# Kernel optimization log

Measured on AMD Instinct MI355X. Metric: run time of the kernel, lower is better.

The kernel has to match this reference:

```python
import jax, jax.numpy as jnp
import numpy as np

IN_F = 512
OUT_F = 512
ALPHA = 0.2   # LeakyReLU negative slope
NEG_INF = -9e15


def setup_inputs() -> dict:
    key = jax.random.key(0)
    k1, k2, k3, k4 = jax.random.split(key, 4)
    B, S = 8, 2048
    hidden_state = jax.random.normal(k1, (B, S, IN_F), dtype=jnp.float32)
    adjacent_matrix = jax.random.uniform(k2, (B, S, S), dtype=jnp.float32)
    # nn.Linear weight (no bias): stored as [out, in] in torch; we keep [in, out] for x @ W
    bound = 1.0 / np.sqrt(IN_F)
    W = jax.random.uniform(k3, (IN_F, OUT_F), dtype=jnp.float32, minval=-bound, maxval=bound)
    # xavier_uniform with gain=1.414 on a: shape [2*out, 1]
    a_bound = 1.414 * np.sqrt(6.0 / (2 * OUT_F + 1))
    a = jax.random.uniform(k4, (2 * OUT_F, 1), dtype=jnp.float32, minval=-a_bound, maxval=a_bound)
    return {"hidden_state": hidden_state, "adjacent_matrix": adjacent_matrix, "W": W, "a": a}


def reference(hidden_state, adjacent_matrix, W, a):
    # Wh: [B, S, out]
    Wh = jnp.einsum('bsi,io->bso', hidden_state, W)
    # additive attention: Wh1 + Wh2^T -> [B, S, S]
    Wh1 = Wh @ a[:OUT_F, :]            # [B, S, 1]
    Wh2 = Wh @ a[OUT_F:, :]            # [B, S, 1]
    e = Wh1 + jnp.swapaxes(Wh2, 1, 2)  # [B, S, S]
    e = jax.nn.leaky_relu(e, negative_slope=ALPHA)
    attention = jnp.where(adjacent_matrix > 0.5, e, NEG_INF)
    # NOTE: original softmaxes over dim=1 (the *row* index), faithfully reproduced
    attention = jax.nn.softmax(attention, axis=1)
    # dropout is identity at inference (training=False)
    h_prime = jnp.einsum('bst,bto->bso', attention, Wh)
    return jax.nn.elu(h_prime)  # concat=True path
```

## Files before the change

### kernel.cpp

```cpp
#include <hip/hip_runtime.h>
#include <hip/hip_bf16.h>
#include <stdint.h>

#define SDIM 2048
#define BDIM 8
#define FDIM 512
constexpr float ALPHA = 0.2f;

typedef __attribute__((ext_vector_type(8))) short bf16x8;
typedef __attribute__((ext_vector_type(4))) float f32x4;

__device__ __forceinline__ unsigned short f2bf(float x) {
  __hip_bfloat16 h = __float2bfloat16(x);
  return *reinterpret_cast<unsigned short*>(&h);
}

__device__ __forceinline__ void gload_lds16(const void* g, void* l) {
  __builtin_amdgcn_global_load_lds(
      (const __attribute__((address_space(1))) unsigned int*)(uintptr_t)g,
      (__attribute__((address_space(3))) unsigned int*)(uintptr_t)l,
      16, 0, 0);
}

__global__ void k0_prep(const float* __restrict__ W, const float* __restrict__ a,
                        float* __restrict__ wa, __hip_bfloat16* __restrict__ WT) {
  int i = blockIdx.x;
  int lane = threadIdx.x;
  float s1 = 0.f, s2 = 0.f;
  for (int o = lane; o < FDIM; o += 64) {
    float w = W[i * FDIM + o];
    s1 += w * a[o];
    s2 += w * a[FDIM + o];
    WT[o * FDIM + i] = __float2bfloat16(w);
  }
  #pragma unroll
  for (int off = 32; off > 0; off >>= 1) {
    s1 += __shfl_down(s1, off);
    s2 += __shfl_down(s2, off);
  }
  if (lane == 0) { wa[i] = s1; wa[FDIM + i] = s2; }
}

__global__ __launch_bounds__(256) void k1_rows(const float* __restrict__ H,
                                               const float* __restrict__ wa,
                                               float* __restrict__ Wh1, float* __restrict__ Wh2,
                                               __hip_bfloat16* __restrict__ Hb) {
  int wid = threadIdx.x >> 6, lane = threadIdx.x & 63;
  long r = (long)blockIdx.x * 4 + wid;
  const float* hr = H + r * FDIM;
  float4 v0 = ((const float4*)hr)[lane];
  float4 v1 = ((const float4*)hr)[lane + 64];
  float4 wa10 = ((const float4*)wa)[lane];
  float4 wa11 = ((const float4*)wa)[lane + 64];
  float4 wa20 = ((const float4*)(wa + FDIM))[lane];
  float4 wa21 = ((const float4*)(wa + FDIM))[lane + 64];
  float s1 = v0.x*wa10.x + v0.y*wa10.y + v0.z*wa10.z + v0.w*wa10.w
           + v1.x*wa11.x + v1.y*wa11.y + v1.z*wa11.z + v1.w*wa11.w;
  float s2 = v0.x*wa20.x + v0.y*wa20.y + v0.z*wa20.z + v0.w*wa20.w
           + v1.x*wa21.x + v1.y*wa21.y + v1.z*wa21.z + v1.w*wa21.w;
  ushort4 u0 = { f2bf(v0.x), f2bf(v0.y), f2bf(v0.z), f2bf(v0.w) };
  ushort4 u1 = { f2bf(v1.x), f2bf(v1.y), f2bf(v1.z), f2bf(v1.w) };
  ushort4* hb = (ushort4*)(Hb + r * FDIM);
  hb[lane] = u0;
  hb[lane + 64] = u1;
  #pragma unroll
  for (int off = 32; off > 0; off >>= 1) {
    s1 += __shfl_down(s1, off);
    s2 += __shfl_down(s2, off);
  }
  if (lane == 0) { Wh1[r] = s1; Wh2[r] = s2; }
}

__global__ __launch_bounds__(256) void k2_z(const float* __restrict__ adj,
                                            const float* __restrict__ Wh1,
                                            const float* __restrict__ Wh2,
                                            float* __restrict__ Zp) {
  int t = blockIdx.x * 256 + threadIdx.x;
  int b = blockIdx.y;
  int c = blockIdx.z;
  float w2 = Wh2[b * SDIM + t];
  const float* arow = adj + ((long)b * SDIM + c * 64) * SDIM + t;
  const float* w1p = Wh1 + b * SDIM + c * 64;
  float z = 0.f;
  #pragma unroll 8
  for (int s = 0; s < 64; ++s) {
    float av = arow[(long)s * SDIM];
    float e = w1p[s] + w2;
    e = e > 0.f ? e : ALPHA * e;
    float p = __expf(e);
    z += (av > 0.5f) ? p : 0.f;
  }
  Zp[(b * 32 + c) * SDIM + t] = z;
}

__global__ void k2b_rz(const float* __restrict__ Zp, float* __restrict__ rZ) {
  int idx = blockIdx.x * 256 + threadIdx.x;
  int b = idx >> 11, t = idx & 2047;
  float z = 0.f;
  #pragma unroll
  for (int c = 0; c < 32; ++c) z += Zp[(b * 32 + c) * SDIM + t];
  rZ[idx] = 1.0f / z;
}

__global__ __launch_bounds__(256) void k3_gemm(const __hip_bfloat16* __restrict__ WTm,
                                               const __hip_bfloat16* __restrict__ Hb,
                                               const float* __restrict__ rZ,
                                               __hip_bfloat16* __restrict__ VT) {
  __shared__ __align__(16) __hip_bfloat16 Asm[2][128 * 32];
  __shared__ __align__(16) __hip_bfloat16 Bsm[2][128 * 32];
  const int o0 = blockIdx.x * 128;
  const int t0 = blockIdx.y * 128;
  const int b = blockIdx.z;
  const int tid = threadIdx.x;
  const int w = tid >> 6, lane = tid & 63;
  const int wm = w >> 1, wn = w & 1;
  const int fr = lane & 15, fq = lane >> 4;
  const int lr = lane >> 2, lb = (lane & 3) * 16;

  const __hip_bfloat16* Abase = WTm + (long)o0 * FDIM;
  const __hip_bfloat16* Bbase = Hb + ((long)b * SDIM + t0) * FDIM;

  f32x4 acc[4][4] = {};

  auto stage = [&](int kk, int buf) {
    #pragma unroll
    for (int g = 0; g < 2; ++g) {
      int rbase = g * 64 + w * 16;
      int row = rbase + lr;
      gload_lds16((const char*)(Abase + (long)row * FDIM + kk * 32) + lb,
                  (char*)&Asm[buf][0] + rbase * 64);
      gload_lds16((const char*)(Bbase + (long)row * FDIM + kk * 32) + lb,
                  (char*)&Bsm[buf][0] + rbase * 64);
    }
  };

  stage(0, 0);
  __syncthreads();
  for (int kk = 0; kk < 16; ++kk) {
    int cur = kk & 1;
    if (kk < 15) stage(kk + 1, cur ^ 1);
    bf16x8 af[4], bf_[4];
    #pragma unroll
    for (int mf = 0; mf < 4; ++mf)
      af[mf] = *(const bf16x8*)((const char*)&Asm[cur][0] + (wm * 64 + mf * 16 + fr) * 64 + fq * 16);
    #pragma unroll
    for (int nf = 0; nf < 4; ++nf)
      bf_[nf] = *(const bf16x8*)((const char*)&Bsm[cur][0] + (wn * 64 + nf * 16 + fr) * 64 + fq * 16);
    #pragma unroll
    for (int mf = 0; mf < 4; ++mf)
      #pragma unroll
      for (int nf = 0; nf < 4; ++nf)
        acc[mf][nf] = __builtin_amdgcn_mfma_f32_16x16x32_bf16(af[mf], bf_[nf], acc[mf][nf], 0, 0, 0);
    __syncthreads();
  }

  #pragma unroll
  for (int nf = 0; nf < 4; ++nf) {
    int t = t0 + wn * 64 + nf * 16 + fr;
    float rz = rZ[b * SDIM + t];
    #pragma unroll
    for (int mf = 0; mf < 4; ++mf) {
      #pragma unroll
      for (int r = 0; r < 4; ++r) {
        int o = o0 + wm * 64 + mf * 16 + fq * 4 + r;
        VT[((long)(b * FDIM + o)) * SDIM + t] = __float2bfloat16(acc[mf][nf][r] * rz);
      }
    }
  }
}

__global__ __launch_bounds__(256, 2) void k4_pv(const float* __restrict__ adj,
                                                const float* __restrict__ Wh1,
                                                const float* __restrict__ Wh2,
                                                const __hip_bfloat16* __restrict__ VT,
                                                float* __restrict__ out) {
  __shared__ __align__(16) __hip_bfloat16 Psm[2][64 * 32];
  __shared__ __align__(16) float w2l[SDIM];
  const int b  = blockIdx.x;
  const int s0 = blockIdx.y * 64;
  const int ob = blockIdx.z * 256;
  const int tid = threadIdx.x;
  const int w = tid >> 6, lane = tid & 63;
  const int fr = lane & 15, fq = lane >> 4;

  const float w1 = Wh1[b * SDIM + s0 + w * 16 + fr];
  const float* adjR = adj + ((long)(b * SDIM + s0 + w * 16 + fr)) * SDIM;
  const __hip_bfloat16* vbase = VT + ((long)(b * FDIM + ob + w * 64 + fr)) * SDIM;

  f32x4 acc[4][4] = {};

  auto loadA = [&](int pp, float4& a0, float4& a1) {
    const float* s = adjR + pp * 32 + fq * 8;
    a0 = *(const float4*)s;
    a1 = *(const float4*)(s + 4);
  };
  auto build = [&](int pp, int pbuf, const float4& a0, const float4& a1) {
    const float* wrow = &w2l[pp * 32 + fq * 8];
    float4 q0 = *(const float4*)(wrow);
    float4 q1 = *(const float4*)(wrow + 4);
    float aa[8] = {a0.x,a0.y,a0.z,a0.w,a1.x,a1.y,a1.z,a1.w};
    float qq[8] = {q0.x,q0.y,q0.z,q0.w,q1.x,q1.y,q1.z,q1.w};
    bf16x8 pv;
    #pragma unroll
    for (int i = 0; i < 8; ++i) {
      float e = w1 + qq[i];
      e = fmaxf(e, ALPHA * e);
      float pr = (aa[i] > 0.5f) ? __expf(e) : 0.f;
      pv[i] = (short)f2bf(pr);
    }
    *(bf16x8*)((char*)&Psm[pbuf][0] + w * 1024 + lane * 16) = pv;
  };

  {
    const float* src = Wh2 + (long)b * SDIM + tid * 8;
    float4 t0 = *(const float4*)(src);
    float4 t1 = *(const float4*)(src + 4);
    *(float4*)(&w2l[tid * 8]) = t0;
    *(float4*)(&w2l[tid * 8 + 4]) = t1;
  }
  float4 a0A, a1A, a0B, a1B, a0C, a1C, a0D, a1D;
  loadA(0, a0A, a1A);
  loadA(1, a0B, a1B);
  loadA(2, a0C, a1C);
  __syncthreads();
  build(0, 0, a0A, a1A);
  asm volatile("s_waitcnt lgkmcnt(0)" ::: "memory");
  __builtin_amdgcn_sched_barrier(0);
  __builtin_amdgcn_s_barrier();

  auto phase = [&](int p, const float4& c0, const float4& c1, float4& f0, float4& f1) {
    const int cur = p & 1;
    bf16x8 vb[4];
    #pragma unroll
    for (int nf = 0; nf < 4; ++nf)
      vb[nf] = *(const bf16x8*)(vbase + (long)nf * 16 * SDIM + p * 32 + fq * 8);
    if (p + 3 < 64) loadA(p + 3, f0, f1);
    __builtin_amdgcn_sched_barrier(0);
    bf16x8 pa[4];
    #pragma unroll
    for (int mf = 0; mf < 4; ++mf)
      pa[mf] = *(const bf16x8*)((const char*)&Psm[cur][0] + mf * 1024 + lane * 16);
    if (p + 1 < 64) build(p + 1, cur ^ 1, c0, c1);
    __builtin_amdgcn_sched_barrier(0);
    __builtin_amdgcn_s_setprio(1);
    #pragma unroll
    for (int mf = 0; mf < 4; ++mf)
      #pragma unroll
      for (int nf = 0; nf < 4; ++nf)
        acc[mf][nf] = __builtin_amdgcn_mfma_f32_16x16x32_bf16(pa[mf], vb[nf], acc[mf][nf], 0, 0, 0);
    __builtin_amdgcn_s_setprio(0);
    asm volatile("s_waitcnt lgkmcnt(0)" ::: "memory");
    __builtin_amdgcn_sched_barrier(0);
    __builtin_amdgcn_s_barrier();
  };

  for (int j = 0; j < 16; ++j) {
    phase(4 * j + 0, a0B, a1B, a0D, a1D);
    phase(4 * j + 1, a0C, a1C, a0A, a1A);
    phase(4 * j + 2, a0D, a1D, a0B, a1B);
    phase(4 * j + 3, a0A, a1A, a0C, a1C);
  }

  float* orow = out + ((long)b * SDIM + s0) * FDIM + ob + w * 64;
  #pragma unroll
  for (int mf = 0; mf < 4; ++mf) {
    #pragma unroll
    for (int nf = 0; nf < 4; ++nf) {
      #pragma unroll
      for (int r = 0; r < 4; ++r) {
        int s = mf * 16 + fq * 4 + r;
        int o = nf * 16 + fr;
        float x = acc[mf][nf][r];
        x = x > 0.f ? x : (__expf(x) - 1.f);
        orow[(long)s * FDIM + o] = x;
      }
    }
  }
}

extern "C" void kernel_launch(void* const* d_in, const int* in_sizes, int n_in,
                              void* d_out, int out_size, void* d_ws, size_t ws_size,
                              hipStream_t stream) {
  const float* H   = (const float*)d_in[0];
  const float* adj = (const float*)d_in[1];
  const float* W   = (const float*)d_in[2];
  const float* a   = (const float*)d_in[3];
  float* out = (float*)d_out;
  char* ws = (char*)d_ws;

  __hip_bfloat16* VT  = (__hip_bfloat16*)(ws + 0);
  __hip_bfloat16* Hb  = (__hip_bfloat16*)(ws + 16777216);
  __hip_bfloat16* WT  = (__hip_bfloat16*)(ws + 33554432);
  float* wa  = (float*)(ws + 34078720);
  float* Wh1 = (float*)(ws + 34082816);
  float* Wh2 = (float*)(ws + 34148352);
  float* rZ  = (float*)(ws + 34213888);
  float* Zp  = (float*)(ws + 34279424);

  hipLaunchKernelGGL(k0_prep, dim3(512), dim3(64), 0, stream, W, a, wa, WT);
  hipLaunchKernelGGL(k1_rows, dim3(4096), dim3(256), 0, stream, H, wa, Wh1, Wh2, Hb);
  hipLaunchKernelGGL(k2_z, dim3(8, 8, 32), dim3(256), 0, stream, adj, Wh1, Wh2, Zp);
  hipLaunchKernelGGL(k2b_rz, dim3(64), dim3(256), 0, stream, Zp, rZ);
  hipLaunchKernelGGL(k3_gemm, dim3(4, 16, 8), dim3(256), 0, stream, WT, Hb, rZ, VT);
  hipLaunchKernelGGL(k4_pv, dim3(8, 32, 2), dim3(256), 0, stream, adj, Wh1, Wh2, VT, out);
}
```

Before: 148.5 us.

## Halve k4_pv row tile to 32 rows, doubling blocks and raising occupancy

The P·V kernel now processes 32 query rows per block instead of 64, which doubles the grid to 1024 blocks and raises launch bounds to 4 blocks per SM. The P-tile build is remapped so each thread computes 4 probabilities for a 32x32 tile, with a new shared-memory layout. The goal is more parallelism and better latency hiding on the adjacency-bound stream. The cost is that each VT tile is reused across only 32 rows, so VT traffic doubles and the w2l staging is repeated in twice as many blocks.

New measurement: 186.5 us. +25.6%, slower.

```diff
diff --git a/kernel.cpp b/kernel.cpp
--- a/kernel.cpp
+++ b/kernel.cpp
@@ -169,46 +169,45 @@
   }
 }
 
-__global__ __launch_bounds__(256, 2) void k4_pv(const float* __restrict__ adj,
+__global__ __launch_bounds__(256, 4) void k4_pv(const float* __restrict__ adj,
                                                 const float* __restrict__ Wh1,
                                                 const float* __restrict__ Wh2,
                                                 const __hip_bfloat16* __restrict__ VT,
                                                 float* __restrict__ out) {
-  __shared__ __align__(16) __hip_bfloat16 Psm[2][64 * 32];
+  __shared__ __align__(16) __hip_bfloat16 Psm[2][32 * 32];
   __shared__ __align__(16) float w2l[SDIM];
   const int b  = blockIdx.x;
-  const int s0 = blockIdx.y * 64;
+  const int s0 = blockIdx.y * 32;
   const int ob = blockIdx.z * 256;
   const int tid = threadIdx.x;
   const int w = tid >> 6, lane = tid & 63;
   const int fr = lane & 15, fq = lane >> 4;
-
-  const float w1 = Wh1[b * SDIM + s0 + w * 16 + fr];
-  const float* adjR = adj + ((long)(b * SDIM + s0 + w * 16 + fr)) * SDIM;
+  const int bfq = tid & 3, bh = (tid >> 2) & 1;
+  const int bfr = (tid >> 3) & 15, bmf = tid >> 7;
+  const int brow = bmf * 16 + bfr;
+
+  const float w1 = Wh1[b * SDIM + s0 + brow];
+  const float* adjR = adj + ((long)(b * SDIM + s0 + brow)) * SDIM;
   const __hip_bfloat16* vbase = VT + ((long)(b * FDIM + ob + w * 64 + fr)) * SDIM;
 
-  f32x4 acc[4][4] = {};
-
-  auto loadA = [&](int pp, float4& a0, float4& a1) {
-    const float* s = adjR + pp * 32 + fq * 8;
-    a0 = *(const float4*)s;
-    a1 = *(const float4*)(s + 4);
+  f32x4 acc[2][4] = {};
+
+  auto loadA = [&](int pp, float4& a0) {
+    a0 = *(const float4*)(adjR + pp * 32 + bfq * 8 + bh * 4);
   };
-  auto build = [&](int pp, int pbuf, const float4& a0, const float4& a1) {
-    const float* wrow = &w2l[pp * 32 + fq * 8];
-    float4 q0 = *(const float4*)(wrow);
-    float4 q1 = *(const float4*)(wrow + 4);
-    float aa[8] = {a0.x,a0.y,a0.z,a0.w,a1.x,a1.y,a1.z,a1.w};
-    float qq[8] = {q0.x,q0.y,q0.z,q0.w,q1.x,q1.y,q1.z,q1.w};
-    bf16x8 pv;
-    #pragma unroll
-    for (int i = 0; i < 8; ++i) {
+  auto build = [&](int pp, int pbuf, const float4& a0) {
+    float4 q0 = *(const float4*)(&w2l[pp * 32 + bfq * 8 + bh * 4]);
+    float aa[4] = {a0.x, a0.y, a0.z, a0.w};
+    float qq[4] = {q0.x, q0.y, q0.z, q0.w};
+    ushort4 pv;
+    #pragma unroll
+    for (int i = 0; i < 4; ++i) {
       float e = w1 + qq[i];
       e = fmaxf(e, ALPHA * e);
       float pr = (aa[i] > 0.5f) ? __expf(e) : 0.f;
-      pv[i] = (short)f2bf(pr);
+      ((unsigned short*)&pv)[i] = f2bf(pr);
     }
-    *(bf16x8*)((char*)&Psm[pbuf][0] + w * 1024 + lane * 16) = pv;
+    *(ushort4*)((char*)&Psm[pbuf][0] + bmf * 1024 + bfr * 64 + bfq * 16 + bh * 8) = pv;
   };
 
   {
@@ -218,33 +217,33 @@
     *(float4*)(&w2l[tid * 8]) = t0;
     *(float4*)(&w2l[tid * 8 + 4]) = t1;
   }
-  float4 a0A, a1A, a0B, a1B, a0C, a1C, a0D, a1D;
-  loadA(0, a0A, a1A);
-  loadA(1, a0B, a1B);
-  loadA(2, a0C, a1C);
+  float4 aA, aB, aC, aD;
+  loadA(0, aA);
+  loadA(1, aB);
+  loadA(2, aC);
   __syncthreads();
-  build(0, 0, a0A, a1A);
+  build(0, 0, aA);
   asm volatile("s_waitcnt lgkmcnt(0)" ::: "memory");
   __builtin_amdgcn_sched_barrier(0);
   __builtin_amdgcn_s_barrier();
 
-  auto phase = [&](int p, const float4& c0, const float4& c1, float4& f0, float4& f1) {
+  auto phase = [&](int p, const float4& c0, float4& f0) {
     const int cur = p & 1;
     bf16x8 vb[4];
     #pragma unroll
     for (int nf = 0; nf < 4; ++nf)
       vb[nf] = *(const bf16x8*)(vbase + (long)nf * 16 * SDIM + p * 32 + fq * 8);
-    if (p + 3 < 64) loadA(p + 3, f0, f1);
+    if (p + 3 < 64) loadA(p + 3, f0);
     __builtin_amdgcn_sched_barrier(0);
-    bf16x8 pa[4];
-    #pragma unroll
-    for (int mf = 0; mf < 4; ++mf)
-      pa[mf] = *(const bf16x8*)((const char*)&Psm[cur][0] + mf * 1024 + lane * 16);
-    if (p + 1 < 64) build(p + 1, cur ^ 1, c0, c1);
+    bf16x8 pa[2];
+    #pragma unroll
+    for (int mf = 0; mf < 2; ++mf)
+      pa[mf] = *(const bf16x8*)((const char*)&Psm[cur][0] + mf * 1024 + fr * 64 + fq * 16);
+    if (p + 1 < 64) build(p + 1, cur ^ 1, c0);
     __builtin_amdgcn_sched_barrier(0);
     __builtin_amdgcn_s_setprio(1);
     #pragma unroll
-    for (int mf = 0; mf < 4; ++mf)
+    for (int mf = 0; mf < 2; ++mf)
       #pragma unroll
       for (int nf = 0; nf < 4; ++nf)
         acc[mf][nf] = __builtin_amdgcn_mfma_f32_16x16x32_bf16(pa[mf], vb[nf], acc[mf][nf], 0, 0, 0);
@@ -255,15 +254,15 @@
   };
 
   for (int j = 0; j < 16; ++j) {
-    phase(4 * j + 0, a0B, a1B, a0D, a1D);
-    phase(4 * j + 1, a0C, a1C, a0A, a1A);
-    phase(4 * j + 2, a0D, a1D, a0B, a1B);
-    phase(4 * j + 3, a0A, a1A, a0C, a1C);
+    phase(4 * j + 0, aB, aD);
+    phase(4 * j + 1, aC, aA);
+    phase(4 * j + 2, aD, aB);
+    phase(4 * j + 3, aA, aC);
   }
 
   float* orow = out + ((long)b * SDIM + s0) * FDIM + ob + w * 64;
   #pragma unroll
-  for (int mf = 0; mf < 4; ++mf) {
+  for (int mf = 0; mf < 2; ++mf) {
     #pragma unroll
     for (int nf = 0; nf < 4; ++nf) {
       #pragma unroll
@@ -302,5 +301,5 @@
   hipLaunchKernelGGL(k2_z, dim3(8, 8, 32), dim3(256), 0, stream, adj, Wh1, Wh2, Zp);
   hipLaunchKernelGGL(k2b_rz, dim3(64), dim3(256), 0, stream, Zp, rZ);
   hipLaunchKernelGGL(k3_gemm, dim3(4, 16, 8), dim3(256), 0, stream, WT, Hb, rZ, VT);
-  hipLaunchKernelGGL(k4_pv, dim3(8, 32, 2), dim3(256), 0, stream, adj, Wh1, Wh2, VT, out);
-}
+  hipLaunchKernelGGL(k4_pv, dim3(8, 64, 2), dim3(256), 0, stream, adj, Wh1, Wh2, VT, out);
+}
```
